# Kernel optimization log

Measured on AMD Instinct MI355X. Metric: run time of the kernel, lower is better.

Reference implementation:

```python
import jax, jax.numpy as jnp
import numpy as np

N = 100000   # nodes
E = 1250000  # edges
R = 8        # num_relations
D = 64       # in_channels = hidden = out dim (all 64 per RGIN_Net construction)
L = 2        # max_depth
EPS = 1e-5


def setup_inputs() -> dict:
    key = jax.random.key(0)
    ks = jax.random.split(key, 18)
    s = 1.0 / np.sqrt(D)
    inp = {
        'x': jax.random.normal(ks[0], (N, D), dtype=jnp.float32),
        'edge_index': jax.random.randint(ks[1], (2, E), 0, N, dtype=jnp.int64),
        'edge_type': jax.random.randint(ks[2], (E,), 0, R, dtype=jnp.int64),
        # per-relation MLP params, stacked over L layers and R relations
        'W1': jax.random.normal(ks[3], (L, R, D, D), dtype=jnp.float32) * s,
        'b1': jax.random.normal(ks[4], (L, R, D), dtype=jnp.float32) * 0.01,
        'g1': 1.0 + 0.1 * jax.random.normal(ks[5], (L, R, D), dtype=jnp.float32),
        'be1': jax.random.normal(ks[6], (L, R, D), dtype=jnp.float32) * 0.01,
        'W2': jax.random.normal(ks[7], (L, R, D, D), dtype=jnp.float32) * s,
        'b2': jax.random.normal(ks[8], (L, R, D), dtype=jnp.float32) * 0.01,
        # root MLP params per layer
        'rW1': jax.random.normal(ks[9], (L, D, D), dtype=jnp.float32) * s,
        'rb1': jax.random.normal(ks[10], (L, D), dtype=jnp.float32) * 0.01,
        'rg1': 1.0 + 0.1 * jax.random.normal(ks[11], (L, D), dtype=jnp.float32),
        'rbe1': jax.random.normal(ks[12], (L, D), dtype=jnp.float32) * 0.01,
        'rW2': jax.random.normal(ks[13], (L, D, D), dtype=jnp.float32) * s,
        'rb2': jax.random.normal(ks[14], (L, D), dtype=jnp.float32) * 0.01,
        'bias': jax.random.normal(ks[15], (L, D), dtype=jnp.float32) * 0.01,
    }
    return inp


def _bn(z, gamma, beta, axis):
    # BatchNorm1d in training mode: batch stats, biased variance
    mean = jnp.mean(z, axis=axis, keepdims=True)
    var = jnp.mean(jnp.square(z - mean), axis=axis, keepdims=True)
    return (z - mean) * jax.lax.rsqrt(var + EPS) * gamma + beta


def _forward(x, edge_index, edge_type, W1, b1, g1, be1, W2, b2,
             rW1, rb1, rg1, rbe1, rW2, rb2, bias):
    src, dst = edge_index[0], edge_index[1]
    # combined segment id encodes (relation, dst-node) -> one fused scatter-add
    seg = edge_type * N + dst
    for i in range(L):
        # gather -> scatter-add per relation: h[r, n] = sum_{e: type=r, dst=n} x[src[e]]
        h = jax.ops.segment_sum(x[src], seg, num_segments=R * N).reshape(R, N, D)
        # per-relation MLP: Linear -> BN -> ReLU -> Linear (summed over relations)
        z = jnp.einsum('rnd,rdh->rnh', h, W1[i]) + b1[i][:, None, :]
        z = jax.nn.relu(_bn(z, g1[i][:, None, :], be1[i][:, None, :], axis=1))
        rel = jnp.einsum('rnh,rho->rno', z, W2[i]) + b2[i][:, None, :]
        out = rel.sum(axis=0)
        # root MLP on x itself
        zr = x @ rW1[i] + rb1[i]
        zr = jax.nn.relu(_bn(zr, rg1[i], rbe1[i], axis=0))
        out = out + zr @ rW2[i] + rb2[i] + bias[i]
        x = jax.nn.relu(out) if i + 1 < L else out  # dropout p=0.0
    return x


def reference(x, edge_index, edge_type, W1, b1, g1, be1, W2, b2,
              rW1, rb1, rg1, rbe1, rW2, rb2, bias):
    return _forward(x, edge_index, edge_type, W1, b1, g1, be1, W2, b2,
                    rW1, rb1, rg1, rbe1, rW2, rb2, bias)
```

## Files before the change

### kernel.cpp

```cpp
#include <hip/hip_runtime.h>

#define NN 100000
#define NE 1250000
#define NR 8
#define DD 64
#define TILE 128
#define NTILES 782
#define NBUCKETS (NR * NTILES)
#define CAP 512
#define HROW 72
#define EPSB 1e-5f

typedef unsigned short u16;
typedef unsigned int u32;
typedef __attribute__((ext_vector_type(8))) short short8;
typedef __attribute__((ext_vector_type(4))) float f32x4;

static __device__ __forceinline__ float b2f_lo(u32 v) { return __uint_as_float(v << 16); }
static __device__ __forceinline__ float b2f_hi(u32 v) { return __uint_as_float(v & 0xffff0000u); }
static __device__ __forceinline__ u16 f2b(float f) {
    u32 u = __float_as_uint(f);
    u += 0x7fffu + ((u >> 16) & 1u);
    return (u16)(u >> 16);
}
static __device__ __forceinline__ u32 pk(float a, float b) {
    return (u32)f2b(a) | ((u32)f2b(b) << 16);
}
static __device__ __forceinline__ void acc8(float* acc, uint4 v0, uint4 v1, uint4 v2, uint4 v3) {
#pragma unroll
    for (int q = 0; q < 4; q++) {
        uint4 v = (q == 0) ? v0 : (q == 1) ? v1 : (q == 2) ? v2 : v3;
        acc[q * 8 + 0] += b2f_lo(v.x);
        acc[q * 8 + 1] += b2f_hi(v.x);
        acc[q * 8 + 2] += b2f_lo(v.y);
        acc[q * 8 + 3] += b2f_hi(v.y);
        acc[q * 8 + 4] += b2f_lo(v.z);
        acc[q * 8 + 5] += b2f_hi(v.z);
        acc[q * 8 + 6] += b2f_lo(v.w);
        acc[q * 8 + 7] += b2f_hi(v.w);
    }
}


__global__ void cvt_kernel(const float* __restrict__ in, u16* __restrict__ outb) {
    int i = blockIdx.x * 256 + threadIdx.x;
    if (i < NN * DD / 8) {
        float4 a = *(const float4*)&in[i * 8];
        float4 b = *(const float4*)&in[i * 8 + 4];
        uint4 o;
        o.x = pk(a.x, a.y); o.y = pk(a.z, a.w);
        o.z = pk(b.x, b.y); o.w = pk(b.z, b.w);
        *(uint4*)&outb[i * 8] = o;
    }
}


__global__ void wt_kernel(const float* __restrict__ W1, const float* __restrict__ rW1,
                          const float* __restrict__ W2, const float* __restrict__ rW2,
                          u16* __restrict__ wt1g, u16* __restrict__ wt2g) {
    int m = blockIdx.x;
    int i = m / 18, rest = m % 18;
    int set = rest / 9, r = rest % 9;
    const float* W = (set == 0)
        ? ((r < NR) ? (W1 + ((size_t)i * NR + r) * DD * DD) : (rW1 + (size_t)i * DD * DD))
        : ((r < NR) ? (W2 + ((size_t)i * NR + r) * DD * DD) : (rW2 + (size_t)i * DD * DD));
    u32* dst = (u32*)((set == 0 ? wt1g : wt2g) + ((size_t)i * 9 + r) * DD * DD);
    for (int j = threadIdx.x; j < DD * 32; j += 256) {
        int d = j >> 5, kp = j & 31;
        dst[j] = pk(W[(2 * kp) * DD + d], W[(2 * kp + 1) * DD + d]);
    }
}


__global__ void count_kernel(const int* __restrict__ dst,
                             const int* __restrict__ et,
                             int* __restrict__ cnt) {
    int i = blockIdx.x * 256 + threadIdx.x;
    if (i < NE) atomicAdd(&cnt[et[i] * NTILES + (dst[i] >> 7)], 1);
}

__global__ void scan_kernel(const int* __restrict__ cnt, int* __restrict__ off, int n) {
    __shared__ int ts[1024];
    int t = threadIdx.x;
    int v[8];
    int s = 0;
#pragma unroll
    for (int j = 0; j < 8; j++) {
        int idx = t * 8 + j;
        int c = (idx < n) ? cnt[idx] : 0;
        v[j] = s;
        s += c;
    }
    ts[t] = s;
    __syncthreads();
    for (int d = 1; d < 1024; d <<= 1) {
        int add = (t >= d) ? ts[t - d] : 0;
        __syncthreads();
        ts[t] += add;
        __syncthreads();
    }
    int base = (t > 0) ? ts[t - 1] : 0;
#pragma unroll
    for (int j = 0; j < 8; j++) {
        int idx = t * 8 + j;
        if (idx < n) off[idx] = base + v[j];
    }
    if (t == 1023) off[n] = ts[1023];
}

__global__ void fill_kernel(const int* __restrict__ src, const int* __restrict__ dst,
                            const int* __restrict__ et, const int* __restrict__ off,
                            int* __restrict__ cursor, int* __restrict__ ep) {
    int i = blockIdx.x * 256 + threadIdx.x;
    if (i < NE) {
        int d = dst[i];
        int b = et[i] * NTILES + (d >> 7);
        int pos = off[b] + atomicAdd(&cursor[b], 1);
        ep[pos] = (src[i] << 8) | (d & 127);
    }
}


__launch_bounds__(256, 4)
__global__ void gemm1_kernel(const u16* __restrict__ xb,
                             const int* __restrict__ ep, const int* __restrict__ off,
                             const u16* __restrict__ wt1, const float* __restrict__ b1l,
                             const float* __restrict__ rb1l,
                             u16* __restrict__ zb, float* __restrict__ stats) {
    __shared__ u16 hsb[TILE * HROW];
    __shared__ int seS[CAP], seD[CAP];
    __shared__ int shist[TILE], scur[TILE];
    __shared__ int soff[TILE + 1];
    __shared__ float red[2 * DD];
    int r = blockIdx.y;
    bool root = (r == NR);
    int n0 = blockIdx.x * TILE;
    int tid = threadIdx.x;

    int wv = tid >> 6;
    int l  = tid & 63;
    int lr = l & 15;
    int lg = l >> 4;

    if (tid < 128) red[tid] = 0.f;

    if (!root) {
        int b = r * NTILES + blockIdx.x;
        int e0 = off[b], e1 = off[b + 1];
        int m = e1 - e0;
        int slot = tid & 127, half = tid >> 7;
        float acc[32];
#pragma unroll
        for (int j = 0; j < 32; j++) acc[j] = 0.f;

        for (int base = 0; base < m; base += CAP) {
            int cnt = min(m - base, CAP);
            if (tid < TILE) shist[tid] = 0;
            __syncthreads();
            for (int i = tid; i < cnt; i += 256) {
                int p = ep[e0 + base + i];
                seS[i] = p;
                atomicAdd(&shist[p & 127], 1);
            }
            __syncthreads();
            if (tid < 64) {
                int c0 = shist[tid], c1 = shist[tid + 64];
                int s0 = c0, s1 = c1;
#pragma unroll
                for (int d = 1; d < 64; d <<= 1) {
                    int t0 = __shfl_up(s0, d);
                    int t1 = __shfl_up(s1, d);
                    if (tid >= d) { s0 += t0; s1 += t1; }
                }
                int tot0 = __shfl(s0, 63);
                soff[tid + 1]  = s0;
                soff[tid + 65] = tot0 + s1;
                if (tid == 0) soff[0] = 0;
                scur[tid]      = s0 - c0;
                scur[tid + 64] = tot0 + s1 - c1;
            }
            __syncthreads();
            for (int i = tid; i < cnt; i += 256) {
                int p = seS[i];
                seD[atomicAdd(&scur[p & 127], 1)] = p;
            }
            __syncthreads();
            int sb = soff[slot], se = soff[slot + 1];
            int e = sb;
            for (; e + 2 <= se; e += 2) {
                const u16* xr0 = &xb[(size_t)(seD[e] >> 8) * DD + half * 32];
                const u16* xr1 = &xb[(size_t)(seD[e + 1] >> 8) * DD + half * 32];
                uint4 a0 = *(const uint4*)(xr0);      uint4 c0 = *(const uint4*)(xr1);
                uint4 a1 = *(const uint4*)(xr0 + 8);  uint4 c1 = *(const uint4*)(xr1 + 8);
                uint4 a2 = *(const uint4*)(xr0 + 16); uint4 c2 = *(const uint4*)(xr1 + 16);
                uint4 a3 = *(const uint4*)(xr0 + 24); uint4 c3 = *(const uint4*)(xr1 + 24);
                acc8(acc, a0, a1, a2, a3);
                acc8(acc, c0, c1, c2, c3);
            }
            if (e < se) {
                const u16* xr = &xb[(size_t)(seD[e] >> 8) * DD + half * 32];
                acc8(acc, *(const uint4*)(xr), *(const uint4*)(xr + 8),
                     *(const uint4*)(xr + 16), *(const uint4*)(xr + 24));
            }
        }
        u32 pw[16];
#pragma unroll
        for (int j = 0; j < 16; j++) pw[j] = pk(acc[2 * j], acc[2 * j + 1]);
        u16* hrow = &hsb[slot * HROW + half * 32];
        *(uint4*)(hrow)      = make_uint4(pw[0], pw[1], pw[2], pw[3]);
        *(uint4*)(hrow + 8)  = make_uint4(pw[4], pw[5], pw[6], pw[7]);
        *(uint4*)(hrow + 16) = make_uint4(pw[8], pw[9], pw[10], pw[11]);
        *(uint4*)(hrow + 24) = make_uint4(pw[12], pw[13], pw[14], pw[15]);
    } else {
        for (int idx = tid; idx < TILE * 8; idx += 256) {
            int row = idx >> 3, q = idx & 7;
            int n = n0 + row;
            uint4 v = make_uint4(0, 0, 0, 0);
            if (n < NN) v = *(const uint4*)&xb[(size_t)n * DD + q * 8];
            *(uint4*)&hsb[row * HROW + q * 8] = v;
        }
    }

    const u16* wtg = wt1 + (size_t)r * DD * DD;
    short8 bfrg[2][4];
#pragma unroll
    for (int ks = 0; ks < 2; ks++)
#pragma unroll
        for (int ct = 0; ct < 4; ct++)
            bfrg[ks][ct] = *(const short8*)&wtg[(ct * 16 + lr) * DD + ks * 32 + lg * 8];
    __syncthreads();

    f32x4 dacc[2][4];
#pragma unroll
    for (int rt = 0; rt < 2; rt++)
#pragma unroll
        for (int ct = 0; ct < 4; ct++) dacc[rt][ct] = (f32x4){0.f, 0.f, 0.f, 0.f};

#pragma unroll
    for (int ks = 0; ks < 2; ks++) {
        short8 afr[2];
#pragma unroll
        for (int rt = 0; rt < 2; rt++)
            afr[rt] = *(const short8*)&hsb[(wv * 32 + rt * 16 + lr) * HROW + ks * 32 + lg * 8];
#pragma unroll
        for (int ct = 0; ct < 4; ct++) {
            dacc[0][ct] = __builtin_amdgcn_mfma_f32_16x16x32_bf16(afr[0], bfrg[ks][ct], dacc[0][ct], 0, 0, 0);
            dacc[1][ct] = __builtin_amdgcn_mfma_f32_16x16x32_bf16(afr[1], bfrg[ks][ct], dacc[1][ct], 0, 0, 0);
        }
    }

    const float* bvec = root ? rb1l : (b1l + r * DD);
    float bv4[4], s1v[4], s2v[4];
#pragma unroll
    for (int ct = 0; ct < 4; ct++) { bv4[ct] = bvec[16 * ct + lr]; s1v[ct] = 0.f; s2v[ct] = 0.f; }
#pragma unroll
    for (int rt = 0; rt < 2; rt++)
#pragma unroll
        for (int ct = 0; ct < 4; ct++)
#pragma unroll
            for (int i = 0; i < 4; i++) {
                float v = dacc[rt][ct][i] + bv4[ct];
                dacc[rt][ct][i] = v;
                int n = n0 + wv * 32 + rt * 16 + lg * 4 + i;
                if (n < NN) { s1v[ct] += v; s2v[ct] += v * v; }
            }
#pragma unroll
    for (int ct = 0; ct < 4; ct++) {
        float a = s1v[ct], bq = s2v[ct];
        a += __shfl_xor(a, 16); bq += __shfl_xor(bq, 16);
        a += __shfl_xor(a, 32); bq += __shfl_xor(bq, 32);
        if (lg == 0) {
            atomicAdd(&red[16 * ct + lr], a);
            atomicAdd(&red[64 + 16 * ct + lr], bq);
        }
    }
    __syncthreads();

#pragma unroll
    for (int rt = 0; rt < 2; rt++)
#pragma unroll
        for (int ct = 0; ct < 4; ct++)
#pragma unroll
            for (int i = 0; i < 4; i++)
                hsb[(wv * 32 + rt * 16 + lg * 4 + i) * HROW + 16 * ct + lr] = f2b(dacc[rt][ct][i]);
    __syncthreads();

    u16* zout = zb + (size_t)r * NN * DD;
    for (int idx = tid; idx < TILE * 8; idx += 256) {
        int row = idx >> 3, q = idx & 7;
        int n = n0 + row;
        if (n < NN)
            *(uint4*)&zout[(size_t)n * DD + q * 8] = *(const uint4*)&hsb[row * HROW + q * 8];
    }
    if (tid < 64) {
        atomicAdd(&stats[r * DD + tid], red[tid]);
        atomicAdd(&stats[576 + r * DD + tid], red[64 + tid]);
    }
}


__global__ void finalize_kernel(const float* __restrict__ stats,
                                const float* __restrict__ g1l, const float* __restrict__ be1l,
                                const float* __restrict__ rg1l, const float* __restrict__ rbe1l,
                                const float* __restrict__ b2l, const float* __restrict__ rb2l,
                                const float* __restrict__ biasl,
                                float* __restrict__ affine, float* __restrict__ constd) {
    int t = threadIdx.x;
    if (t < 576) {
        int r = t >> 6, d = t & 63;
        float mean = stats[t] * (1.f / NN);
        float var = fmaxf(stats[576 + t] * (1.f / NN) - mean * mean, 0.f);
        float g  = (r < NR) ? g1l[r * DD + d]  : rg1l[d];
        float be = (r < NR) ? be1l[r * DD + d] : rbe1l[d];
        float sc = g * rsqrtf(var + EPSB);
        affine[t] = sc;
        affine[576 + t] = be - mean * sc;
        if (r == 0) {
            float cd = rb2l[d] + biasl[d];
#pragma unroll
            for (int rr = 0; rr < NR; rr++) cd += b2l[rr * DD + d];
            constd[d] = cd;
        }
    }
}


__launch_bounds__(256, 4)
__global__ void pass2_kernel(const u16* __restrict__ zb, const u16* __restrict__ wt2,
                             const float* __restrict__ affine, const float* __restrict__ constd,
                             float* __restrict__ outf, u16* __restrict__ outb,
                             int emit_bf16_relu) {
    __shared__ u16 zsb[TILE * HROW];
    __shared__ u16 wtb[DD * HROW];
    int n0 = blockIdx.x * TILE;
    int tid = threadIdx.x;
    int srow = tid >> 3;
    int sc0 = (tid & 7) * 8;

    int wv = tid >> 6;
    int l  = tid & 63;
    int lr = l & 15;
    int lg = l >> 4;

    f32x4 dacc[2][4];
#pragma unroll
    for (int rt = 0; rt < 2; rt++)
#pragma unroll
        for (int ct = 0; ct < 4; ct++) dacc[rt][ct] = (f32x4){0.f, 0.f, 0.f, 0.f};

    uint4 preA[4], preB[4];
    u32 wreg[8];
#pragma unroll
    for (int q = 0; q < 4; q++) {
        int n = n0 + srow + 32 * q;
        preA[q] = (n < NN) ? *(const uint4*)&zb[(size_t)n * DD + sc0] : make_uint4(0, 0, 0, 0);
        preB[q] = (n < NN) ? *(const uint4*)&zb[(size_t)NN * DD + (size_t)n * DD + sc0]
                           : make_uint4(0, 0, 0, 0);
    }
    {
        const u32* wsrc = (const u32*)wt2;
#pragma unroll
        for (int j = 0; j < 8; j++) wreg[j] = wsrc[tid + 256 * j];
    }

#pragma unroll
    for (int r = 0; r < 9; r++) {
        uint4* cur = (r & 1) ? preB : preA;
        float4 aLo = *(const float4*)&affine[r * DD + sc0];
        float4 aHi = *(const float4*)&affine[r * DD + sc0 + 4];
        float4 cLo = *(const float4*)&affine[576 + r * DD + sc0];
        float4 cHi = *(const float4*)&affine[576 + r * DD + sc0 + 4];
        __syncthreads();
#pragma unroll
        for (int q = 0; q < 4; q++) {
            uint4 vv = cur[q];
            float a0 = fmaxf(fmaf(b2f_lo(vv.x), aLo.x, cLo.x), 0.f);
            float a1 = fmaxf(fmaf(b2f_hi(vv.x), aLo.y, cLo.y), 0.f);
            float a2 = fmaxf(fmaf(b2f_lo(vv.y), aLo.z, cLo.z), 0.f);
            float a3 = fmaxf(fmaf(b2f_hi(vv.y), aLo.w, cLo.w), 0.f);
            float a4 = fmaxf(fmaf(b2f_lo(vv.z), aHi.x, cHi.x), 0.f);
            float a5 = fmaxf(fmaf(b2f_hi(vv.z), aHi.y, cHi.y), 0.f);
            float a6 = fmaxf(fmaf(b2f_lo(vv.w), aHi.z, cHi.z), 0.f);
            float a7 = fmaxf(fmaf(b2f_hi(vv.w), aHi.w, cHi.w), 0.f);
            uint4 o = make_uint4(pk(a0, a1), pk(a2, a3), pk(a4, a5), pk(a6, a7));
            *(uint4*)&zsb[(srow + 32 * q) * HROW + sc0] = o;
        }
        {
            int row = tid >> 5, q = tid & 31;
#pragma unroll
            for (int j = 0; j < 8; j++)
                ((u32*)&wtb[(row + 8 * j) * HROW])[q] = wreg[j];
        }
        __syncthreads();
        if (r + 1 < 9) {
            const u32* wsrc = (const u32*)(wt2 + (size_t)(r + 1) * DD * DD);
#pragma unroll
            for (int j = 0; j < 8; j++) wreg[j] = wsrc[tid + 256 * j];
        }
        if (r + 2 < 9) {
            const u16* zp = zb + (size_t)(r + 2) * NN * DD;
#pragma unroll
            for (int q = 0; q < 4; q++) {
                int n = n0 + srow + 32 * q;
                cur[q] = (n < NN) ? *(const uint4*)&zp[(size_t)n * DD + sc0]
                                  : make_uint4(0, 0, 0, 0);
            }
        }
#pragma unroll
        for (int ks = 0; ks < 2; ks++) {
            short8 afr[2];
#pragma unroll
            for (int rt = 0; rt < 2; rt++)
                afr[rt] = *(const short8*)&zsb[(wv * 32 + rt * 16 + lr) * HROW + ks * 32 + lg * 8];
#pragma unroll
            for (int ct = 0; ct < 4; ct++) {
                short8 bfr = *(const short8*)&wtb[(ct * 16 + lr) * HROW + ks * 32 + lg * 8];
                dacc[0][ct] = __builtin_amdgcn_mfma_f32_16x16x32_bf16(afr[0], bfr, dacc[0][ct], 0, 0, 0);
                dacc[1][ct] = __builtin_amdgcn_mfma_f32_16x16x32_bf16(afr[1], bfr, dacc[1][ct], 0, 0, 0);
            }
        }
    }

    float cd4[4];
#pragma unroll
    for (int ct = 0; ct < 4; ct++) cd4[ct] = constd[16 * ct + lr];

    if (emit_bf16_relu) {
        __syncthreads();
#pragma unroll
        for (int rt = 0; rt < 2; rt++)
#pragma unroll
            for (int ct = 0; ct < 4; ct++)
#pragma unroll
                for (int i = 0; i < 4; i++) {
                    float v = fmaxf(dacc[rt][ct][i] + cd4[ct], 0.f);
                    zsb[(wv * 32 + rt * 16 + lg * 4 + i) * HROW + 16 * ct + lr] = f2b(v);
                }
        __syncthreads();
        for (int idx = tid; idx < TILE * 8; idx += 256) {
            int row = idx >> 3, q = idx & 7;
            int n = n0 + row;
            if (n < NN)
                *(uint4*)&outb[(size_t)n * DD + q * 8] = *(const uint4*)&zsb[row * HROW + q * 8];
        }
    } else {
        float* zf = (float*)zsb;
#pragma unroll
        for (int h = 0; h < 2; h++) {
            __syncthreads();
#pragma unroll
            for (int rt = 0; rt < 2; rt++)
#pragma unroll
                for (int cc = 0; cc < 2; cc++) {
                    int ct = 2 * h + cc;
#pragma unroll
                    for (int i = 0; i < 4; i++)
                        zf[(wv * 32 + rt * 16 + lg * 4 + i) * 34 + 16 * cc + lr] =
                            dacc[rt][ct][i] + cd4[ct];
                }
            __syncthreads();
            for (int idx = tid; idx < TILE * 8; idx += 256) {
                int row = idx >> 3, q = idx & 7;
                int n = n0 + row;
                if (n < NN)
                    *(float4*)&outf[(size_t)n * DD + 32 * h + q * 4] =
                        *(const float4*)&zf[row * 34 + q * 4];
            }
        }
    }
}


extern "C" void kernel_launch(void* const* d_in, const int* in_sizes, int n_in,
                              void* d_out, int out_size, void* d_ws, size_t ws_size,
                              hipStream_t stream) {
    (void)in_sizes; (void)n_in; (void)out_size;

    const float* x0   = (const float*)d_in[0];
    const int*   ei   = (const int*)d_in[1];
    const int*   et   = (const int*)d_in[2];
    const float* W1   = (const float*)d_in[3];
    const float* b1   = (const float*)d_in[4];
    const float* g1   = (const float*)d_in[5];
    const float* be1  = (const float*)d_in[6];
    const float* W2   = (const float*)d_in[7];
    const float* b2   = (const float*)d_in[8];
    const float* rW1  = (const float*)d_in[9];
    const float* rb1  = (const float*)d_in[10];
    const float* rg1  = (const float*)d_in[11];
    const float* rbe1 = (const float*)d_in[12];
    const float* rW2  = (const float*)d_in[13];
    const float* rb2  = (const float*)d_in[14];
    const float* bias = (const float*)d_in[15];
    float* out = (float*)d_out;

    char* ws = (char*)d_ws;
    size_t zelems = (size_t)9 * NN * DD;
    u16* zb   = (u16*)ws;
    u16* xb   = zb + zelems;
    u16* wt1g = xb + (size_t)NN * DD;
    u16* wt2g = wt1g + 18 * DD * DD;
    float* stats  = (float*)(wt2g + 18 * DD * DD);
    float* affine = stats + 1152;
    float* constd = affine + 1152;
    int* cnt    = (int*)(constd + 64);
    int* cursor = cnt + NBUCKETS;
    int* off    = cursor + NBUCKETS;
    int* ep     = off + NBUCKETS + 1;

    size_t need = (zelems + (size_t)NN * DD + 36 * DD * DD) * 2
                + (1152 + 1152 + 64) * 4
                + ((size_t)3 * NBUCKETS + 1 + NE) * 4;
    if (ws_size < need) return;

    cvt_kernel<<<(NN * DD / 8 + 255) / 256, 256, 0, stream>>>(x0, xb);
    wt_kernel<<<36, 256, 0, stream>>>(W1, rW1, W2, rW2, wt1g, wt2g);
    hipMemsetAsync(cnt, 0, sizeof(int) * 2 * NBUCKETS, stream);
    count_kernel<<<(NE + 255) / 256, 256, 0, stream>>>(ei + NE, et, cnt);
    scan_kernel<<<1, 1024, 0, stream>>>(cnt, off, NBUCKETS);
    fill_kernel<<<(NE + 255) / 256, 256, 0, stream>>>(ei, ei + NE, et, off, cursor, ep);

    for (int i = 0; i < 2; i++) {
        hipMemsetAsync(stats, 0, sizeof(float) * 1152, stream);
        gemm1_kernel<<<dim3(NTILES, 9), 256, 0, stream>>>(
            xb, ep, off,
            wt1g + (size_t)i * 9 * DD * DD,
            b1 + (size_t)i * NR * DD, rb1 + (size_t)i * DD,
            zb, stats);
        finalize_kernel<<<1, 576, 0, stream>>>(
            stats,
            g1 + (size_t)i * NR * DD, be1 + (size_t)i * NR * DD,
            rg1 + (size_t)i * DD, rbe1 + (size_t)i * DD,
            b2 + (size_t)i * NR * DD, rb2 + (size_t)i * DD, bias + (size_t)i * DD,
            affine, constd);
        pass2_kernel<<<NTILES, 256, 0, stream>>>(
            zb, wt2g + (size_t)i * 9 * DD * DD,
            affine, constd, out, xb, (i == 0) ? 1 : 0);
    }
}
```

Before: 452.3 us.

## Presort edges by (relation, dst) globally; drop in-kernel LDS bucketing; add nontemporal z I/O

Edge preprocessing now builds a full CSR keyed by (relation, dst node) with a per-node count, a per-bucket scan and a fill pass. gemm1 can then read each node's source list straight from global memory instead of re-bucketing edges in LDS with atomics and several barriers on every layer. The change also frees shared memory for better occupancy and uses nontemporal loads and stores for the large z buffer and the output. The cost is extra preprocessing kernels, more atomic traffic on a larger counter array, and a bigger memset, all paid once rather than per layer.

After: 514.3 us. +13.7%, slower.

```diff
diff --git a/kernel.cpp b/kernel.cpp
--- a/kernel.cpp
+++ b/kernel.cpp
@@ -7,7 +7,7 @@
 #define TILE 128
 #define NTILES 782
 #define NBUCKETS (NR * NTILES)
-#define CAP 512
+#define NB128 (NBUCKETS * 128)
 #define HROW 72
 #define EPSB 1e-5f
 
@@ -15,6 +15,7 @@
 typedef unsigned int u32;
 typedef __attribute__((ext_vector_type(8))) short short8;
 typedef __attribute__((ext_vector_type(4))) float f32x4;
+typedef __attribute__((ext_vector_type(4))) u32 u32x4;
 
 static __device__ __forceinline__ float b2f_lo(u32 v) { return __uint_as_float(v << 16); }
 static __device__ __forceinline__ float b2f_hi(u32 v) { return __uint_as_float(v & 0xffff0000u); }
@@ -25,6 +26,13 @@
 }
 static __device__ __forceinline__ u32 pk(float a, float b) {
     return (u32)f2b(a) | ((u32)f2b(b) << 16);
+}
+static __device__ __forceinline__ void nt_store4(void* p, uint4 v) {
+    __builtin_nontemporal_store(*(u32x4*)&v, (u32x4*)p);
+}
+static __device__ __forceinline__ uint4 nt_load4(const void* p) {
+    u32x4 t = __builtin_nontemporal_load((const u32x4*)p);
+    return *(uint4*)&t;
 }
 static __device__ __forceinline__ void acc8(float* acc, uint4 v0, uint4 v1, uint4 v2, uint4 v3) {
 #pragma unroll
@@ -108,29 +116,54 @@
     if (t == 1023) off[n] = ts[1023];
 }
 
-__global__ void fill_kernel(const int* __restrict__ src, const int* __restrict__ dst,
-                            const int* __restrict__ et, const int* __restrict__ off,
-                            int* __restrict__ cursor, int* __restrict__ ep) {
+__global__ void count2_kernel(const int* __restrict__ dst, const int* __restrict__ et,
+                              int* __restrict__ cnt2) {
     int i = blockIdx.x * 256 + threadIdx.x;
     if (i < NE) {
         int d = dst[i];
-        int b = et[i] * NTILES + (d >> 7);
-        int pos = off[b] + atomicAdd(&cursor[b], 1);
-        ep[pos] = (src[i] << 8) | (d & 127);
+        atomicAdd(&cnt2[(et[i] * NTILES + (d >> 7)) * 128 + (d & 127)], 1);
+    }
+}
+
+__global__ void segscan_kernel(const int* __restrict__ cnt2, const int* __restrict__ off,
+                               int* __restrict__ soffg) {
+    int b = blockIdx.x;
+    int t = threadIdx.x;
+    int i0 = b * 128 + 2 * t;
+    int c0 = cnt2[i0], c1 = cnt2[i0 + 1];
+    int s = c0 + c1;
+    int incl = s;
+#pragma unroll
+    for (int d = 1; d < 64; d <<= 1) {
+        int v = __shfl_up(incl, d);
+        if (t >= d) incl += v;
+    }
+    int start = off[b] + incl - s;
+    soffg[i0] = start;
+    soffg[i0 + 1] = start + c0;
+    if (b == 0 && t == 0) soffg[NB128] = off[NBUCKETS];
+}
+
+__global__ void fill2_kernel(const int* __restrict__ src, const int* __restrict__ dst,
+                             const int* __restrict__ et, const int* __restrict__ soffg,
+                             int* __restrict__ cur, int* __restrict__ ep2) {
+    int i = blockIdx.x * 256 + threadIdx.x;
+    if (i < NE) {
+        int d = dst[i];
+        int idx = (et[i] * NTILES + (d >> 7)) * 128 + (d & 127);
+        int pos = soffg[idx] + atomicAdd(&cur[idx], 1);
+        ep2[pos] = src[i];
     }
 }
 
 
 __launch_bounds__(256, 4)
 __global__ void gemm1_kernel(const u16* __restrict__ xb,
-                             const int* __restrict__ ep, const int* __restrict__ off,
+                             const int* __restrict__ ep2, const int* __restrict__ soffg,
                              const u16* __restrict__ wt1, const float* __restrict__ b1l,
                              const float* __restrict__ rb1l,
                              u16* __restrict__ zb, float* __restrict__ stats) {
     __shared__ u16 hsb[TILE * HROW];
-    __shared__ int seS[CAP], seD[CAP];
-    __shared__ int shist[TILE], scur[TILE];
-    __shared__ int soff[TILE + 1];
     __shared__ float red[2 * DD];
     int r = blockIdx.y;
     bool root = (r == NR);
@@ -145,63 +178,29 @@
     if (tid < 128) red[tid] = 0.f;
 
     if (!root) {
-        int b = r * NTILES + blockIdx.x;
-        int e0 = off[b], e1 = off[b + 1];
-        int m = e1 - e0;
         int slot = tid & 127, half = tid >> 7;
+        int idx = (r * NTILES + blockIdx.x) * 128 + slot;
+        int sb = soffg[idx], se = soffg[idx + 1];
         float acc[32];
 #pragma unroll
         for (int j = 0; j < 32; j++) acc[j] = 0.f;
 
-        for (int base = 0; base < m; base += CAP) {
-            int cnt = min(m - base, CAP);
-            if (tid < TILE) shist[tid] = 0;
-            __syncthreads();
-            for (int i = tid; i < cnt; i += 256) {
-                int p = ep[e0 + base + i];
-                seS[i] = p;
-                atomicAdd(&shist[p & 127], 1);
-            }
-            __syncthreads();
-            if (tid < 64) {
-                int c0 = shist[tid], c1 = shist[tid + 64];
-                int s0 = c0, s1 = c1;
-#pragma unroll
-                for (int d = 1; d < 64; d <<= 1) {
-                    int t0 = __shfl_up(s0, d);
-                    int t1 = __shfl_up(s1, d);
-                    if (tid >= d) { s0 += t0; s1 += t1; }
-                }
-                int tot0 = __shfl(s0, 63);
-                soff[tid + 1]  = s0;
-                soff[tid + 65] = tot0 + s1;
-                if (tid == 0) soff[0] = 0;
-                scur[tid]      = s0 - c0;
-                scur[tid + 64] = tot0 + s1 - c1;
-            }
-            __syncthreads();
-            for (int i = tid; i < cnt; i += 256) {
-                int p = seS[i];
-                seD[atomicAdd(&scur[p & 127], 1)] = p;
-            }
-            __syncthreads();
-            int sb = soff[slot], se = soff[slot + 1];
-            int e = sb;
-            for (; e + 2 <= se; e += 2) {
-                const u16* xr0 = &xb[(size_t)(seD[e] >> 8) * DD + half * 32];
-                const u16* xr1 = &xb[(size_t)(seD[e + 1] >> 8) * DD + half * 32];
-                uint4 a0 = *(const uint4*)(xr0);      uint4 c0 = *(const uint4*)(xr1);
-                uint4 a1 = *(const uint4*)(xr0 + 8);  uint4 c1 = *(const uint4*)(xr1 + 8);
-                uint4 a2 = *(const uint4*)(xr0 + 16); uint4 c2 = *(const uint4*)(xr1 + 16);
-                uint4 a3 = *(const uint4*)(xr0 + 24); uint4 c3 = *(const uint4*)(xr1 + 24);
-                acc8(acc, a0, a1, a2, a3);
-                acc8(acc, c0, c1, c2, c3);
-            }
-            if (e < se) {
-                const u16* xr = &xb[(size_t)(seD[e] >> 8) * DD + half * 32];
-                acc8(acc, *(const uint4*)(xr), *(const uint4*)(xr + 8),
-                     *(const uint4*)(xr + 16), *(const uint4*)(xr + 24));
-            }
+        int e = sb;
+        for (; e + 2 <= se; e += 2) {
+            int s0 = ep2[e], s1 = ep2[e + 1];
+            const u16* xr0 = &xb[(size_t)s0 * DD + half * 32];
+            const u16* xr1 = &xb[(size_t)s1 * DD + half * 32];
+            uint4 a0 = *(const uint4*)(xr0);      uint4 c0 = *(const uint4*)(xr1);
+            uint4 a1 = *(const uint4*)(xr0 + 8);  uint4 c1 = *(const uint4*)(xr1 + 8);
+            uint4 a2 = *(const uint4*)(xr0 + 16); uint4 c2 = *(const uint4*)(xr1 + 16);
+            uint4 a3 = *(const uint4*)(xr0 + 24); uint4 c3 = *(const uint4*)(xr1 + 24);
+            acc8(acc, a0, a1, a2, a3);
+            acc8(acc, c0, c1, c2, c3);
+        }
+        if (e < se) {
+            const u16* xr = &xb[(size_t)ep2[e] * DD + half * 32];
+            acc8(acc, *(const uint4*)(xr), *(const uint4*)(xr + 8),
+                 *(const uint4*)(xr + 16), *(const uint4*)(xr + 24));
         }
         u32 pw[16];
 #pragma unroll
@@ -212,8 +211,8 @@
         *(uint4*)(hrow + 16) = make_uint4(pw[8], pw[9], pw[10], pw[11]);
         *(uint4*)(hrow + 24) = make_uint4(pw[12], pw[13], pw[14], pw[15]);
     } else {
-        for (int idx = tid; idx < TILE * 8; idx += 256) {
-            int row = idx >> 3, q = idx & 7;
+        for (int idx2 = tid; idx2 < TILE * 8; idx2 += 256) {
+            int row = idx2 >> 3, q = idx2 & 7;
             int n = n0 + row;
             uint4 v = make_uint4(0, 0, 0, 0);
             if (n < NN) v = *(const uint4*)&xb[(size_t)n * DD + q * 8];
@@ -286,11 +285,11 @@
     __syncthreads();
 
     u16* zout = zb + (size_t)r * NN * DD;
-    for (int idx = tid; idx < TILE * 8; idx += 256) {
-        int row = idx >> 3, q = idx & 7;
+    for (int idx2 = tid; idx2 < TILE * 8; idx2 += 256) {
+        int row = idx2 >> 3, q = idx2 & 7;
         int n = n0 + row;
         if (n < NN)
-            *(uint4*)&zout[(size_t)n * DD + q * 8] = *(const uint4*)&hsb[row * HROW + q * 8];
+            nt_store4(&zout[(size_t)n * DD + q * 8], *(const uint4*)&hsb[row * HROW + q * 8]);
     }
     if (tid < 64) {
         atomicAdd(&stats[r * DD + tid], red[tid]);
@@ -353,8 +352,8 @@
 #pragma unroll
     for (int q = 0; q < 4; q++) {
         int n = n0 + srow + 32 * q;
-        preA[q] = (n < NN) ? *(const uint4*)&zb[(size_t)n * DD + sc0] : make_uint4(0, 0, 0, 0);
-        preB[q] = (n < NN) ? *(const uint4*)&zb[(size_t)NN * DD + (size_t)n * DD + sc0]
+        preA[q] = (n < NN) ? nt_load4(&zb[(size_t)n * DD + sc0]) : make_uint4(0, 0, 0, 0);
+        preB[q] = (n < NN) ? nt_load4(&zb[(size_t)NN * DD + (size_t)n * DD + sc0])
                            : make_uint4(0, 0, 0, 0);
     }
     {
@@ -402,8 +401,7 @@
 #pragma unroll
             for (int q = 0; q < 4; q++) {
                 int n = n0 + srow + 32 * q;
-                cur[q] = (n < NN) ? *(const uint4*)&zp[(size_t)n * DD + sc0]
-                                  : make_uint4(0, 0, 0, 0);
+                cur[q] = (n < NN) ? nt_load4(&zp[(size_t)n * DD + sc0]) : make_uint4(0, 0, 0, 0);
             }
         }
 #pragma unroll
@@ -463,8 +461,8 @@
                 int row = idx >> 3, q = idx & 7;
                 int n = n0 + row;
                 if (n < NN)
-                    *(float4*)&outf[(size_t)n * DD + 32 * h + q * 4] =
-                        *(const float4*)&zf[row * 34 + q * 4];
+                    nt_store4(&outf[(size_t)n * DD + 32 * h + q * 4],
+                              *(const uint4*)&zf[row * 34 + q * 4]);
             }
         }
     }
@@ -504,26 +502,31 @@
     float* affine = stats + 1152;
     float* constd = affine + 1152;
     int* cnt    = (int*)(constd + 64);
-    int* cursor = cnt + NBUCKETS;
-    int* off    = cursor + NBUCKETS;
-    int* ep     = off + NBUCKETS + 1;
+    int* cnt2   = cnt + NBUCKETS;
+    int* cur2   = cnt2 + NB128;
+    int* off    = cur2 + NB128;
+    int* soffg  = off + NBUCKETS + 1;
+    int* ep2    = soffg + NB128 + 1;
 
     size_t need = (zelems + (size_t)NN * DD + 36 * DD * DD) * 2
                 + (1152 + 1152 + 64) * 4
-                + ((size_t)3 * NBUCKETS + 1 + NE) * 4;
+                + ((size_t)NBUCKETS + 2 * (size_t)NB128 + NBUCKETS + 1
+                   + (size_t)NB128 + 1 + NE) * 4;
     if (ws_size < need) return;
 
     cvt_kernel<<<(NN * DD / 8 + 255) / 256, 256, 0, stream>>>(x0, xb);
     wt_kernel<<<36, 256, 0, stream>>>(W1, rW1, W2, rW2, wt1g, wt2g);
-    hipMemsetAsync(cnt, 0, sizeof(int) * 2 * NBUCKETS, stream);
+    hipMemsetAsync(cnt, 0, sizeof(int) * ((size_t)NBUCKETS + 2 * NB128), stream);
     count_kernel<<<(NE + 255) / 256, 256, 0, stream>>>(ei + NE, et, cnt);
     scan_kernel<<<1, 1024, 0, stream>>>(cnt, off, NBUCKETS);
-    fill_kernel<<<(NE + 255) / 256, 256, 0, stream>>>(ei, ei + NE, et, off, cursor, ep);
+    count2_kernel<<<(NE + 255) / 256, 256, 0, stream>>>(ei + NE, et, cnt2);
+    segscan_kernel<<<NBUCKETS, 64, 0, stream>>>(cnt2, off, soffg);
+    fill2_kernel<<<(NE + 255) / 256, 256, 0, stream>>>(ei, ei + NE, et, soffg, cur2, ep2);
 
     for (int i = 0; i < 2; i++) {
         hipMemsetAsync(stats, 0, sizeof(float) * 1152, stream);
         gemm1_kernel<<<dim3(NTILES, 9), 256, 0, stream>>>(
-            xb, ep, off,
+            xb, ep2, soffg,
             wt1g + (size_t)i * 9 * DD * DD,
             b1 + (size_t)i * NR * DD, rb1 + (size_t)i * DD,
             zb, stats);
```
